# Performance work log

Hardware: AMD Instinct MI355X
Metric: run time of the kernel (lower is better)

The kernel has to match this reference:

```python
import jax, jax.numpy as jnp
import numpy as np

B, S, D, H = 2, 2048, 1024, 16
DK = D // H


def setup_inputs() -> dict:
    key = jax.random.key(0)
    ks = jax.random.split(key, 6)
    scale = 1.0 / np.sqrt(D)
    return {
        "x": jax.random.normal(ks[0], (B, S, D), dtype=jnp.float32),
        "mask": jnp.ones((1, 1, S, S), dtype=jnp.bool_),
        "Wq": jax.random.normal(ks[1], (D, D), dtype=jnp.float32) * scale,
        "bq": jnp.zeros((D,), dtype=jnp.float32),
        "Wk": jax.random.normal(ks[2], (D, D), dtype=jnp.float32) * scale,
        "bk": jnp.zeros((D,), dtype=jnp.float32),
        "Wv": jax.random.normal(ks[3], (D, D), dtype=jnp.float32) * scale,
        "bv": jnp.zeros((D,), dtype=jnp.float32),
        "Wo": jax.random.normal(ks[4], (D, D), dtype=jnp.float32) * scale,
        "bo": jnp.zeros((D,), dtype=jnp.float32),
    }


def reference(x, mask, Wq, bq, Wk, bk, Wv, bv, Wo, bo):
    b, s, d = x.shape
    # projections, split heads: [b, h, s, d_k]
    def proj(W, bias):
        y = jnp.einsum('bsd,de->bse', x, W) + bias
        return y.reshape(b, s, H, DK).transpose(0, 2, 1, 3)
    Q, K, V = proj(Wq, bq), proj(Wk, bk), proj(Wv, bv)
    scores = jnp.einsum('bhqk,bhsk->bhqs', Q, K) / jnp.sqrt(jnp.float32(DK))
    scores = jnp.where(mask, scores, jnp.float32(-jnp.inf))
    attn = jax.nn.softmax(scores, axis=-1)
    ctx = jnp.einsum('bhqs,bhsk->bhqk', attn, V)  # [b,h,s,d_k]
    ctx = ctx.transpose(0, 2, 1, 3).reshape(b, s, d)
    return jnp.einsum('bsd,de->bse', ctx, Wo) + bo
```

## Files before the change

kernel.cpp:

```cpp
#include <hip/hip_runtime.h>
#include <hip/hip_bf16.h>
#include <stdint.h>

#define BB 2
#define SS 2048
#define DDIM 1024
#define HH 16
#define DKH 64
#define MM (BB*SS)
#define QSCALE 0.1803368801111204f

#if __has_builtin(__builtin_amdgcn_exp2f)
#define FAST_EXP2(x) __builtin_amdgcn_exp2f(x)
#else
#define FAST_EXP2(x) exp2f(x)
#endif

typedef __bf16 bf16x8 __attribute__((ext_vector_type(8)));
typedef __bf16 bf16x4 __attribute__((ext_vector_type(4)));
typedef float  f32x4  __attribute__((ext_vector_type(4)));
typedef float  f32x16 __attribute__((ext_vector_type(16)));
typedef uint32_t u32x4 __attribute__((ext_vector_type(4)));
typedef unsigned u32x2 __attribute__((ext_vector_type(2)));

__device__ __forceinline__ void gload_lds16(const void* g, void* l) {
  __builtin_amdgcn_global_load_lds(
      (const __attribute__((address_space(1))) void*)g,
      (__attribute__((address_space(3))) void*)l, 16, 0, 0);
}

__global__ __launch_bounds__(256) void prep_all(
    const float* __restrict__ x, __bf16* __restrict__ xb,
    const float* __restrict__ W0, const float* __restrict__ W1,
    const float* __restrict__ W2, const float* __restrict__ W3,
    __bf16* __restrict__ T0, __bf16* __restrict__ T1,
    __bf16* __restrict__ T2, __bf16* __restrict__ T3) {
  if (blockIdx.z == 4) {
    const int blk = blockIdx.y * 16 + blockIdx.x;
    const size_t base = (size_t)blk * 16384 + threadIdx.x * 4;
#pragma unroll
    for (int it = 0; it < 16; ++it) {
      size_t i = base + (size_t)it * 1024;
      float4 v = *(const float4*)(x + i);
      bf16x4 o;
      o[0] = (__bf16)v.x; o[1] = (__bf16)v.y; o[2] = (__bf16)v.z; o[3] = (__bf16)v.w;
      *(bf16x4*)(xb + i) = o;
    }
    return;
  }
  const float* W; __bf16* T;
  switch (blockIdx.z) {
    case 0: W = W0; T = T0; break;
    case 1: W = W1; T = T1; break;
    case 2: W = W2; T = T2; break;
    default: W = W3; T = T3; break;
  }
  __shared__ float tile[64][65];
  int k0 = blockIdx.x * 64, n0 = blockIdx.y * 64;
  int c = threadIdx.x & 63, r0 = threadIdx.x >> 6;
#pragma unroll
  for (int i = 0; i < 16; ++i) {
    int r = r0 + i * 4;
    tile[r][c] = W[(size_t)(k0 + r) * DDIM + n0 + c];
  }
  __syncthreads();
#pragma unroll
  for (int i = 0; i < 16; ++i) {
    int r = r0 + i * 4;
    T[(size_t)(n0 + r) * DDIM + k0 + c] = (__bf16)tile[c][r];
  }
}

__global__ __launch_bounds__(256) void gemm_qkv(
    const __bf16* __restrict__ A, const __bf16* __restrict__ Bt,
    const float* __restrict__ bq, const float* __restrict__ bk,
    const float* __restrict__ bv,
    __bf16* __restrict__ oq, __bf16* __restrict__ ok, __bf16* __restrict__ ov) {
  __shared__ __align__(16) __bf16 Asm[2][128][64];
  __shared__ __align__(16) __bf16 Bsm[2][128][64];
  const int t = threadIdx.x, lane = t & 63;
  const int w = t >> 6;
  const int bid = blockIdx.y * gridDim.x + blockIdx.x;
  const int xcd = bid & 7, local = bid >> 3;
  const int xm = xcd & 3, xn = xcd >> 2;
  const int m0 = (xm * 8 + (local & 7)) * 128;
  const int n0 = (xn * 12 + (local >> 3)) * 128;
  const int wr = (w >> 1) * 64, wc = (w & 1) * 64;
  const int l15 = lane & 15, lh = lane >> 4;
  f32x4 acc[4][4] = {};

  auto STAGE = [&](int buf, int k0) {
#pragma unroll
    for (int i = 0; i < 4; ++i) {
      int c = i * 256 + t;
      int row = c >> 3;
      int col = ((c & 7) ^ (row & 7)) * 8;
      gload_lds16(A  + (size_t)(m0 + row) * DDIM + k0 + col, &Asm[buf][0][0] + (size_t)c * 8);
      gload_lds16(Bt + (size_t)(n0 + row) * DDIM + k0 + col, &Bsm[buf][0][0] + (size_t)c * 8);
    }
  };

  STAGE(0, 0);
  int cur = 0;
  for (int k0 = 0; k0 < DDIM; k0 += 64) {
    if (k0 + 64 < DDIM) {
      STAGE(cur ^ 1, k0 + 64);
      asm volatile("s_waitcnt vmcnt(8)" ::: "memory");
    } else {
      asm volatile("s_waitcnt vmcnt(0)" ::: "memory");
    }
    __builtin_amdgcn_s_barrier();
#pragma unroll
    for (int kk = 0; kk < 64; kk += 32) {
      bf16x8 af[4], bfr[4];
#pragma unroll
      for (int i = 0; i < 4; ++i) {
        int row = wr + i * 16 + l15;
        af[i]  = *(const bf16x8*)&Asm[cur][row][((((kk >> 3) + lh)) ^ (row & 7)) * 8];
      }
#pragma unroll
      for (int j = 0; j < 4; ++j) {
        int row = wc + j * 16 + l15;
        bfr[j] = *(const bf16x8*)&Bsm[cur][row][((((kk >> 3) + lh)) ^ (row & 7)) * 8];
      }
#pragma unroll
      for (int i = 0; i < 4; ++i)
#pragma unroll
        for (int j = 0; j < 4; ++j)
          acc[i][j] = __builtin_amdgcn_mfma_f32_16x16x32_bf16(af[i], bfr[j], acc[i][j], 0, 0, 0);
    }
    __builtin_amdgcn_s_barrier();
    cur ^= 1;
  }
  const int which = n0 >> 10;
  const float* bias = (which == 0) ? bq : (which == 1) ? bk : bv;
  __bf16* dst = (which == 0) ? oq : (which == 1) ? ok : ov;
  if (which == 2) {
#pragma unroll
    for (int i = 0; i < 4; ++i) {
      int mb = m0 + wr + i * 16 + lh * 4;
      int b = mb >> 11, s0 = mb & (SS - 1);
#pragma unroll
      for (int j = 0; j < 4; ++j) {
        int nl = (n0 & 1023) + wc + j * 16 + l15;
        int h = nl >> 6, dk = nl & (DKH - 1);
        float bv_ = bias[nl];
        bf16x4 pk;
#pragma unroll
        for (int r = 0; r < 4; ++r) pk[r] = (__bf16)(acc[i][j][r] + bv_);
        *(bf16x4*)&dst[((size_t)(b * HH + h) * DKH + dk) * SS + s0] = pk;
      }
    }
  } else {
#pragma unroll
    for (int i = 0; i < 4; ++i)
#pragma unroll
      for (int j = 0; j < 4; ++j)
#pragma unroll
        for (int r = 0; r < 4; ++r) {
          int m = m0 + wr + i * 16 + lh * 4 + r;
          int nl = (n0 & 1023) + wc + j * 16 + l15;
          float v = acc[i][j][r] + bias[nl];
          int b = m >> 11, s = m & (SS - 1);
          int h = nl >> 6, dk = nl & (DKH - 1);
          if (which == 0) v *= QSCALE;
          dst[((size_t)(b * HH + h) * SS + s) * DKH + dk] = (__bf16)v;
        }
  }
}

__global__ __launch_bounds__(256) void gemm_out(
    const __bf16* __restrict__ A, const __bf16* __restrict__ Bt,
    const float* __restrict__ bias, float* __restrict__ out) {
  __shared__ __align__(16) __bf16 Asm[2][64][64];
  __shared__ __align__(16) __bf16 Bsm[2][128][64];
  const int t = threadIdx.x, lane = t & 63;
  const int w = t >> 6;
  const int bid = blockIdx.y * gridDim.x + blockIdx.x;
  const int xcd = bid & 7, local = bid >> 3;
  const int m0 = (xcd * 8 + (local & 7)) * 64;
  const int n0 = (local >> 3) * 128;
  const int wc = w * 32;
  const int l15 = lane & 15, lh = lane >> 4;
  f32x4 acc[4][2] = {};

  auto STAGE = [&](int buf, int k0) {
#pragma unroll
    for (int i = 0; i < 2; ++i) {
      int c = i * 256 + t;
      int row = c >> 3;
      int col = ((c & 7) ^ (row & 7)) * 8;
      gload_lds16(A + (size_t)(m0 + row) * DDIM + k0 + col, &Asm[buf][0][0] + (size_t)c * 8);
    }
#pragma unroll
    for (int i = 0; i < 4; ++i) {
      int c = i * 256 + t;
      int row = c >> 3;
      int col = ((c & 7) ^ (row & 7)) * 8;
      gload_lds16(Bt + (size_t)(n0 + row) * DDIM + k0 + col, &Bsm[buf][0][0] + (size_t)c * 8);
    }
  };

  STAGE(0, 0);
  int cur = 0;
  for (int k0 = 0; k0 < DDIM; k0 += 64) {
    if (k0 + 64 < DDIM) {
      STAGE(cur ^ 1, k0 + 64);
      asm volatile("s_waitcnt vmcnt(6)" ::: "memory");
    } else {
      asm volatile("s_waitcnt vmcnt(0)" ::: "memory");
    }
    __builtin_amdgcn_s_barrier();
#pragma unroll
    for (int kk = 0; kk < 64; kk += 32) {
      bf16x8 af[4], bfr[2];
#pragma unroll
      for (int i = 0; i < 4; ++i) {
        int row = i * 16 + l15;
        af[i]  = *(const bf16x8*)&Asm[cur][row][((((kk >> 3) + lh)) ^ (row & 7)) * 8];
      }
#pragma unroll
      for (int j = 0; j < 2; ++j) {
        int row = wc + j * 16 + l15;
        bfr[j] = *(const bf16x8*)&Bsm[cur][row][((((kk >> 3) + lh)) ^ (row & 7)) * 8];
      }
#pragma unroll
      for (int i = 0; i < 4; ++i)
#pragma unroll
        for (int j = 0; j < 2; ++j)
          acc[i][j] = __builtin_amdgcn_mfma_f32_16x16x32_bf16(af[i], bfr[j], acc[i][j], 0, 0, 0);
    }
    __builtin_amdgcn_s_barrier();
    cur ^= 1;
  }
#pragma unroll
  for (int i = 0; i < 4; ++i)
#pragma unroll
    for (int j = 0; j < 2; ++j)
#pragma unroll
      for (int r = 0; r < 4; ++r) {
        int m = m0 + i * 16 + lh * 4 + r;
        int n = n0 + wc + j * 16 + l15;
        out[(size_t)m * DDIM + n] = acc[i][j][r] + bias[n];
      }
}

__global__ __launch_bounds__(256, 2) void attn_kernel(
    const __bf16* __restrict__ Qb, const __bf16* __restrict__ Kb,
    const __bf16* __restrict__ Vt, __bf16* __restrict__ ctx) {
  __shared__ __align__(16) __bf16 SMEM[4][64][64];
  __shared__ float LmS[256];
  const int t = threadIdx.x, lane = t & 63, w = t >> 6;
  const int l31 = lane & 31, h = lane >> 5;
  const int qh = w & 1, kvh = w >> 1;
  const int work = (blockIdx.x & 7) * 64 + (blockIdx.x >> 3);
  const int bh = work >> 4, qt128 = work & 15;
  const int qbw = qt128 * 128 + qh * 64;
  const __bf16* qptr = Qb + ((size_t)bh * SS + qbw) * DKH;
  const __bf16* kptr = Kb + (size_t)bh * SS * DKH;
  const __bf16* vptr = Vt + (size_t)bh * DKH * SS;

  auto SLOT = [](int row, int s) -> int {
    return row * 64 + ((((s) + (row >> 3)) & 7) ^ (row & 7)) * 8;
  };

  const int c0 = t, c1 = t + 256;
  auto LOADK = [&](int kv0, int c) -> bf16x8 {
    return *(const bf16x8*)(kptr + (size_t)(kv0 + (c >> 3)) * DKH + (c & 7) * 8);
  };
  auto LOADV = [&](int kv0, int c) -> bf16x8 {
    return *(const bf16x8*)(vptr + (size_t)(c >> 3) * SS + kv0 + (c & 7) * 8);
  };
  auto STOREK = [&](int buf, int c, bf16x8 v) {
    *(bf16x8*)(&SMEM[buf][0][0] + SLOT(c >> 3, c & 7)) = v;
  };
  auto STOREV = [&](int buf, int c, bf16x8 v) {
    *(bf16x8*)(&SMEM[2 + buf][0][0] + SLOT(c >> 3, c & 7)) = v;
  };

  auto SMPACK = [&](const f32x16& sv, float& lacc, bf16x8* pa2) {
    float p[16];
#pragma unroll
    for (int i = 0; i < 16; ++i) p[i] = FAST_EXP2(sv[i]);
    lacc += (((p[0] + p[1]) + (p[2] + p[3])) + ((p[4] + p[5]) + (p[6] + p[7])))
          + (((p[8] + p[9]) + (p[10] + p[11])) + ((p[12] + p[13]) + (p[14] + p[15])));
    uint32_t u[8];
#pragma unroll
    for (int i = 0; i < 8; ++i) {
      union { uint32_t v; __bf16 b[2]; } cv;
      cv.b[0] = (__bf16)p[i * 2]; cv.b[1] = (__bf16)p[i * 2 + 1];
      u[i] = cv.v;
    }
    u32x2 r;
    r = __builtin_amdgcn_permlane32_swap(u[0], u[2], false, false); u[0] = r[0]; u[2] = r[1];
    r = __builtin_amdgcn_permlane32_swap(u[1], u[3], false, false); u[1] = r[0]; u[3] = r[1];
    r = __builtin_amdgcn_permlane32_swap(u[4], u[6], false, false); u[4] = r[0]; u[6] = r[1];
    r = __builtin_amdgcn_permlane32_swap(u[5], u[7], false, false); u[5] = r[0]; u[7] = r[1];
    union { u32x4 d; bf16x8 f; } pc;
    pc.d = (u32x4){u[0], u[1], u[2], u[3]}; pa2[0] = pc.f;
    pc.d = (u32x4){u[4], u[5], u[6], u[7]}; pa2[1] = pc.f;
  };

  bf16x8 aq[2][4];
#pragma unroll
  for (int qt = 0; qt < 2; ++qt)
#pragma unroll
    for (int ks = 0; ks < 4; ++ks)
      aq[qt][ks] = *(const bf16x8*)(qptr + (size_t)(qt * 32 + l31) * DKH + ks * 16 + h * 8);

  f32x16 o_acc[2][2] = {};
  float l_run[2] = {0.f, 0.f};

  {
    bf16x8 rk0 = LOADK(0, c0), rk1 = LOADK(0, c1);
    bf16x8 rv0 = LOADV(0, c0), rv1 = LOADV(0, c1);
    STOREK(0, c0, rk0); STOREK(0, c1, rk1);
    STOREV(0, c0, rv0); STOREV(0, c1, rv1);
  }
  __syncthreads();

  int cur = 0;
  for (int kv0 = 0; kv0 < SS; kv0 += 64) {
    const bool more = (kv0 + 64 < SS);
    bf16x8 nk0, nk1, nv0, nv1;
    if (more) {
      nk0 = LOADK(kv0 + 64, c0); nk1 = LOADK(kv0 + 64, c1);
      nv0 = LOADV(kv0 + 64, c0); nv1 = LOADV(kv0 + 64, c1);
    }
    const __bf16* kb_lds = &SMEM[cur][0][0];
    bf16x8 kf[4];
#pragma unroll
    for (int ks = 0; ks < 4; ++ks)
      kf[ks] = *(const bf16x8*)(kb_lds + SLOT(kvh * 32 + l31, ks * 2 + h));
    f32x16 s0 = {}, s1 = {};
    __builtin_amdgcn_s_setprio(1);
#pragma unroll
    for (int ks = 0; ks < 4; ++ks) {
      s0 = __builtin_amdgcn_mfma_f32_32x32x16_bf16(kf[ks], aq[0][ks], s0, 0, 0, 0);
      s1 = __builtin_amdgcn_mfma_f32_32x32x16_bf16(kf[ks], aq[1][ks], s1, 0, 0, 0);
    }
    __builtin_amdgcn_s_setprio(0);
    const __bf16* vb_lds = &SMEM[2 + cur][0][0];
    bf16x8 vf[2][2];
#pragma unroll
    for (int dt = 0; dt < 2; ++dt)
#pragma unroll
      for (int ks = 0; ks < 2; ++ks)
        vf[dt][ks] = *(const bf16x8*)(vb_lds + SLOT(dt * 32 + l31, kvh * 4 + ks * 2 + h));
    bf16x8 pa0[2], pa1[2];
    SMPACK(s0, l_run[0], pa0);
    __builtin_amdgcn_s_setprio(1);
#pragma unroll
    for (int ks = 0; ks < 2; ++ks) {
      o_acc[0][0] = __builtin_amdgcn_mfma_f32_32x32x16_bf16(pa0[ks], vf[0][ks], o_acc[0][0], 0, 0, 0);
      o_acc[0][1] = __builtin_amdgcn_mfma_f32_32x32x16_bf16(pa0[ks], vf[1][ks], o_acc[0][1], 0, 0, 0);
    }
    __builtin_amdgcn_s_setprio(0);
    SMPACK(s1, l_run[1], pa1);
    __builtin_amdgcn_s_setprio(1);
#pragma unroll
    for (int ks = 0; ks < 2; ++ks) {
      o_acc[1][0] = __builtin_amdgcn_mfma_f32_32x32x16_bf16(pa1[ks], vf[0][ks], o_acc[1][0], 0, 0, 0);
      o_acc[1][1] = __builtin_amdgcn_mfma_f32_32x32x16_bf16(pa1[ks], vf[1][ks], o_acc[1][1], 0, 0, 0);
    }
    __builtin_amdgcn_s_setprio(0);
    if (more) {
      STOREK(cur ^ 1, c0, nk0); STOREK(cur ^ 1, c1, nk1);
      STOREV(cur ^ 1, c0, nv0); STOREV(cur ^ 1, c1, nv1);
    }
    __syncthreads();
    cur ^= 1;
  }

#pragma unroll
  for (int qt = 0; qt < 2; ++qt) {
    l_run[qt] += __shfl_xor(l_run[qt], 32, 64);
    if (h == 0) LmS[kvh * 128 + qh * 64 + qt * 32 + l31] = l_run[qt];
  }
  float* Om = (float*)&SMEM[0][0][0];
  if (kvh == 1) {
#pragma unroll
    for (int qt = 0; qt < 2; ++qt)
#pragma unroll
      for (int dt = 0; dt < 2; ++dt)
#pragma unroll
        for (int rg = 0; rg < 4; ++rg) {
          f32x4 v4 = {o_acc[qt][dt][rg * 4], o_acc[qt][dt][rg * 4 + 1],
                      o_acc[qt][dt][rg * 4 + 2], o_acc[qt][dt][rg * 4 + 3]};
          *(f32x4*)&Om[(((((qh * 2 + qt) * 2 + dt) * 4 + rg) * 64) + lane) * 4] = v4;
        }
  }
  __syncthreads();
  if (kvh == 0) {
    const int b = bh >> 4, h16 = bh & 15;
#pragma unroll
    for (int qt = 0; qt < 2; ++qt) {
      float inv = 1.0f / (LmS[qh * 64 + qt * 32 + l31] + LmS[128 + qh * 64 + qt * 32 + l31]);
      float invq[16];
#pragma unroll
      for (int reg = 0; reg < 16; ++reg)
        invq[reg] = __shfl(inv, (reg & 3) + 8 * (reg >> 2) + 4 * h, 64);
#pragma unroll
      for (int dt = 0; dt < 2; ++dt)
#pragma unroll
        for (int rg = 0; rg < 4; ++rg) {
          f32x4 part = *(const f32x4*)&Om[(((((qh * 2 + qt) * 2 + dt) * 4 + rg) * 64) + lane) * 4];
#pragma unroll
          for (int rr = 0; rr < 4; ++rr) {
            int reg = rg * 4 + rr;
            int q = qbw + qt * 32 + (reg & 3) + 8 * (reg >> 2) + 4 * h;
            ctx[((size_t)b * SS + q) * DDIM + h16 * 64 + dt * 32 + l31] =
                (__bf16)((o_acc[qt][dt][reg] + part[rr]) * invq[reg]);
          }
        }
    }
  }
}

extern "C" void kernel_launch(void* const* d_in, const int* in_sizes, int n_in,
                              void* d_out, int out_size, void* d_ws, size_t ws_size,
                              hipStream_t stream) {
  (void)in_sizes; (void)n_in; (void)out_size; (void)ws_size;
  const float* x  = (const float*)d_in[0];
  const float* Wq = (const float*)d_in[2];
  const float* bq = (const float*)d_in[3];
  const float* Wk = (const float*)d_in[4];
  const float* bk = (const float*)d_in[5];
  const float* Wv = (const float*)d_in[6];
  const float* bv = (const float*)d_in[7];
  const float* Wo = (const float*)d_in[8];
  const float* bo = (const float*)d_in[9];
  float* out = (float*)d_out;

  __bf16* xb  = (__bf16*)d_ws;
  __bf16* wtq = xb  + (size_t)MM * DDIM;
  __bf16* wtk = wtq + (size_t)DDIM * DDIM;
  __bf16* wtv = wtk + (size_t)DDIM * DDIM;
  __bf16* wto = wtv + (size_t)DDIM * DDIM;
  __bf16* qb  = wto + (size_t)DDIM * DDIM;
  __bf16* kb  = qb  + (size_t)MM * DDIM;
  __bf16* vtb = kb  + (size_t)MM * DDIM;
  __bf16* ctx = vtb + (size_t)MM * DDIM;

  prep_all<<<dim3(16, 16, 5), 256, 0, stream>>>(x, xb, Wq, Wk, Wv, Wo, wtq, wtk, wtv, wto);
  gemm_qkv<<<dim3(MM / 128, 3 * DDIM / 128), 256, 0, stream>>>(xb, wtq, bq, bk, bv, qb, kb, vtb);
  attn_kernel<<<dim3(BB * HH * (SS / 128)), 256, 0, stream>>>(qb, kb, vtb, ctx);
  gemm_out<<<dim3(MM / 64, DDIM / 128), 256, 0, stream>>>(ctx, wto, bo, out);
}
```

Measured before the change: 111.5 us.

## Widen attention blocks to 512 threads covering 256 queries per block

The attention kernel now uses 8 waves per block, with 4 query groups and 2 KV halves, so each block handles 256 queries instead of 128. Each K/V tile in LDS is shared by twice as many query rows, which halves the global K/V traffic and the per-thread load count. A separate 64KB LDS buffer holds the partial-output reduction because the K/V buffers are too small for it. The grid shrinks to 256 blocks, and the larger LDS footprint plus launch_bounds(512,1) may reduce occupancy and leave CUs underused.

New measurement: 107.5 us (median of 2 runs). 3.6% less time.

```diff
diff --git a/kernel.cpp b/kernel.cpp
--- a/kernel.cpp
+++ b/kernel.cpp
@@ -245,17 +245,18 @@
       }
 }
 
-__global__ __launch_bounds__(256, 2) void attn_kernel(
+__global__ __launch_bounds__(512, 1) void attn_kernel(
     const __bf16* __restrict__ Qb, const __bf16* __restrict__ Kb,
     const __bf16* __restrict__ Vt, __bf16* __restrict__ ctx) {
   __shared__ __align__(16) __bf16 SMEM[4][64][64];
-  __shared__ float LmS[256];
+  __shared__ float LmS[2][256];
+  __shared__ float Om2[16384];
   const int t = threadIdx.x, lane = t & 63, w = t >> 6;
   const int l31 = lane & 31, h = lane >> 5;
-  const int qh = w & 1, kvh = w >> 1;
-  const int work = (blockIdx.x & 7) * 64 + (blockIdx.x >> 3);
-  const int bh = work >> 4, qt128 = work & 15;
-  const int qbw = qt128 * 128 + qh * 64;
+  const int qh = w & 3, kvh = w >> 2;
+  const int work = (blockIdx.x & 7) * 32 + (blockIdx.x >> 3);
+  const int bh = work >> 3, qt256 = work & 7;
+  const int qbw = qt256 * 256 + qh * 64;
   const __bf16* qptr = Qb + ((size_t)bh * SS + qbw) * DKH;
   const __bf16* kptr = Kb + (size_t)bh * SS * DKH;
   const __bf16* vptr = Vt + (size_t)bh * DKH * SS;
@@ -264,18 +265,17 @@
     return row * 64 + ((((s) + (row >> 3)) & 7) ^ (row & 7)) * 8;
   };
 
-  const int c0 = t, c1 = t + 256;
-  auto LOADK = [&](int kv0, int c) -> bf16x8 {
-    return *(const bf16x8*)(kptr + (size_t)(kv0 + (c >> 3)) * DKH + (c & 7) * 8);
-  };
-  auto LOADV = [&](int kv0, int c) -> bf16x8 {
-    return *(const bf16x8*)(vptr + (size_t)(c >> 3) * SS + kv0 + (c & 7) * 8);
-  };
-  auto STOREK = [&](int buf, int c, bf16x8 v) {
-    *(bf16x8*)(&SMEM[buf][0][0] + SLOT(c >> 3, c & 7)) = v;
-  };
-  auto STOREV = [&](int buf, int c, bf16x8 v) {
-    *(bf16x8*)(&SMEM[2 + buf][0][0] + SLOT(c >> 3, c & 7)) = v;
+  auto LOADK = [&](int kv0) -> bf16x8 {
+    return *(const bf16x8*)(kptr + (size_t)(kv0 + (t >> 3)) * DKH + (t & 7) * 8);
+  };
+  auto LOADV = [&](int kv0) -> bf16x8 {
+    return *(const bf16x8*)(vptr + (size_t)(t >> 3) * SS + kv0 + (t & 7) * 8);
+  };
+  auto STOREK = [&](int buf, bf16x8 v) {
+    *(bf16x8*)(&SMEM[buf][0][0] + SLOT(t >> 3, t & 7)) = v;
+  };
+  auto STOREV = [&](int buf, bf16x8 v) {
+    *(bf16x8*)(&SMEM[2 + buf][0][0] + SLOT(t >> 3, t & 7)) = v;
   };
 
   auto SMPACK = [&](const f32x16& sv, float& lacc, bf16x8* pa2) {
@@ -312,21 +312,16 @@
   float l_run[2] = {0.f, 0.f};
 
   {
-    bf16x8 rk0 = LOADK(0, c0), rk1 = LOADK(0, c1);
-    bf16x8 rv0 = LOADV(0, c0), rv1 = LOADV(0, c1);
-    STOREK(0, c0, rk0); STOREK(0, c1, rk1);
-    STOREV(0, c0, rv0); STOREV(0, c1, rv1);
+    bf16x8 rk = LOADK(0), rv = LOADV(0);
+    STOREK(0, rk); STOREV(0, rv);
   }
   __syncthreads();
 
   int cur = 0;
   for (int kv0 = 0; kv0 < SS; kv0 += 64) {
     const bool more = (kv0 + 64 < SS);
-    bf16x8 nk0, nk1, nv0, nv1;
-    if (more) {
-      nk0 = LOADK(kv0 + 64, c0); nk1 = LOADK(kv0 + 64, c1);
-      nv0 = LOADV(kv0 + 64, c0); nv1 = LOADV(kv0 + 64, c1);
-    }
+    bf16x8 nk, nv;
+    if (more) { nk = LOADK(kv0 + 64); nv = LOADV(kv0 + 64); }
     const __bf16* kb_lds = &SMEM[cur][0][0];
     bf16x8 kf[4];
 #pragma unroll
@@ -364,10 +359,7 @@
       o_acc[1][1] = __builtin_amdgcn_mfma_f32_32x32x16_bf16(pa1[ks], vf[1][ks], o_acc[1][1], 0, 0, 0);
     }
     __builtin_amdgcn_s_setprio(0);
-    if (more) {
-      STOREK(cur ^ 1, c0, nk0); STOREK(cur ^ 1, c1, nk1);
-      STOREV(cur ^ 1, c0, nv0); STOREV(cur ^ 1, c1, nv1);
-    }
+    if (more) { STOREK(cur ^ 1, nk); STOREV(cur ^ 1, nv); }
     __syncthreads();
     cur ^= 1;
   }
@@ -375,9 +367,8 @@
 #pragma unroll
   for (int qt = 0; qt < 2; ++qt) {
     l_run[qt] += __shfl_xor(l_run[qt], 32, 64);
-    if (h == 0) LmS[kvh * 128 + qh * 64 + qt * 32 + l31] = l_run[qt];
-  }
-  float* Om = (float*)&SMEM[0][0][0];
+    if (h == 0) LmS[kvh][qh * 64 + qt * 32 + l31] = l_run[qt];
+  }
   if (kvh == 1) {
 #pragma unroll
     for (int qt = 0; qt < 2; ++qt)
@@ -387,7 +378,7 @@
         for (int rg = 0; rg < 4; ++rg) {
           f32x4 v4 = {o_acc[qt][dt][rg * 4], o_acc[qt][dt][rg * 4 + 1],
                       o_acc[qt][dt][rg * 4 + 2], o_acc[qt][dt][rg * 4 + 3]};
-          *(f32x4*)&Om[(((((qh * 2 + qt) * 2 + dt) * 4 + rg) * 64) + lane) * 4] = v4;
+          *(f32x4*)&Om2[((((qh * 2 + qt) * 2 + dt) * 4 + rg) * 64 + lane) * 4] = v4;
         }
   }
   __syncthreads();
@@ -395,7 +386,7 @@
     const int b = bh >> 4, h16 = bh & 15;
 #pragma unroll
     for (int qt = 0; qt < 2; ++qt) {
-      float inv = 1.0f / (LmS[qh * 64 + qt * 32 + l31] + LmS[128 + qh * 64 + qt * 32 + l31]);
+      float inv = 1.0f / (LmS[0][qh * 64 + qt * 32 + l31] + LmS[1][qh * 64 + qt * 32 + l31]);
       float invq[16];
 #pragma unroll
       for (int reg = 0; reg < 16; ++reg)
@@ -404,7 +395,7 @@
       for (int dt = 0; dt < 2; ++dt)
 #pragma unroll
         for (int rg = 0; rg < 4; ++rg) {
-          f32x4 part = *(const f32x4*)&Om[(((((qh * 2 + qt) * 2 + dt) * 4 + rg) * 64) + lane) * 4];
+          f32x4 part = *(const f32x4*)&Om2[((((qh * 2 + qt) * 2 + dt) * 4 + rg) * 64 + lane) * 4];
 #pragma unroll
           for (int rr = 0; rr < 4; ++rr) {
             int reg = rg * 4 + rr;
@@ -444,6 +435,6 @@
 
   prep_all<<<dim3(16, 16, 5), 256, 0, stream>>>(x, xb, Wq, Wk, Wv, Wo, wtq, wtk, wtv, wto);
   gemm_qkv<<<dim3(MM / 128, 3 * DDIM / 128), 256, 0, stream>>>(xb, wtq, bq, bk, bv, qb, kb, vtb);
-  attn_kernel<<<dim3(BB * HH * (SS / 128)), 256, 0, stream>>>(qb, kb, vtb, ctx);
+  attn_kernel<<<dim3(BB * HH * (SS / 256)), 512, 0, stream>>>(qb, kb, vtb, ctx);
   gemm_out<<<dim3(MM / 64, DDIM / 128), 256, 0, stream>>>(ctx, wto, bo, out);
 }
```
